# Kernel tuning notes

Measured on AMD Instinct MI355X. Metric: run time of the kernel, lower is better.

## Reference

```python
import jax, jax.numpy as jnp
import numpy as np
from itertools import combinations

DIM = 3
METRIC = np.array([1.0, 1.0, 1.0], dtype=np.float32)
KERNEL_SIZE = 7
C_IN, C_OUT = 32, 32
HIDDEN = 64
NUM_LAYERS = 4
N_GRID = KERNEL_SIZE ** DIM


def _build_cayley(dim, metric):
    blades = [()] + [c for r in range(1, dim + 1) for c in combinations(range(dim), r)]
    idx = {b: i for i, b in enumerate(blades)}
    n = len(blades)
    C = np.zeros((n, n, n), dtype=np.float32)
    for i, a in enumerate(blades):
        for j, b in enumerate(blades):
            arr = list(a) + list(b)
            sign = 1.0
            changed = True
            while changed:
                changed = False
                t = 0
                while t < len(arr) - 1:
                    if arr[t] == arr[t + 1]:
                        sign *= metric[arr[t]]
                        del arr[t:t + 2]
                        changed = True
                        break
                    if arr[t] > arr[t + 1]:
                        arr[t], arr[t + 1] = arr[t + 1], arr[t]
                        sign = -sign
                        changed = True
                    t += 1
            C[i, j, idx[tuple(arr)]] = sign
    grades = np.array([len(b) for b in blades])
    return C, grades

_C_LRO, GRADES = _build_cayley(DIM, METRIC)
CAYLEY = np.transpose(_C_LRO, (0, 2, 1))  # [left, out, right] (CEGNN convention)
N_BLADES = CAYLEY.shape[0]
N_GRADES = DIM + 1

# nonzero grade-triple paths of the Cayley tensor and blade-level path-id lookup
_gp = np.zeros((N_GRADES,) * 3, dtype=bool)
for a in range(N_GRADES):
    for b in range(N_GRADES):
        for c in range(N_GRADES):
            _gp[a, b, c] = np.any(CAYLEY[np.ix_(GRADES == a, GRADES == b, GRADES == c)] != 0)
PATHS = np.argwhere(_gp)
P = len(PATHS)
assert P == 20  # product_paths_sum for Cl(3,0)
_pid = -np.ones((N_GRADES,) * 3, dtype=np.int64)
for p, (a, b, c) in enumerate(PATHS):
    _pid[a, b, c] = p
BLADE_PID = _pid[GRADES[:, None, None], GRADES[None, :, None], GRADES[None, None, :]]
BLADE_PID = np.where(BLADE_PID < 0, P, BLADE_PID)  # P -> zero slot

# centered relative-position grid, (N, 1, dim)
_ax = np.arange(KERNEL_SIZE, dtype=np.float32) - (KERNEL_SIZE - 1) / 2.0
_grid = np.stack(np.meshgrid(*([_ax] * DIM), indexing='ij'), axis=-1).reshape(-1, DIM)
REL_POS = jnp.asarray(_grid[:, None, :])
CAYLEY_J = jnp.asarray(CAYLEY)
GRADE_ONEHOT = jnp.asarray((GRADES[:, None] == np.arange(N_GRADES)[None, :]).astype(np.float32))
FACTOR = 1.0 / np.sqrt(float(KERNEL_SIZE ** DIM))
BLADES_OF = {g: np.where(GRADES == g)[0] for g in range(N_GRADES)}


def embed_grade(x, g):
    out = jnp.zeros(x.shape[:-1] + (N_BLADES,), x.dtype)
    return out.at[..., BLADES_OF[g]].set(x)


def expand_paths(w):
    # (..., P) grade-path weights -> (..., B, B, B) blade-level weights
    wz = jnp.concatenate([w, jnp.zeros(w.shape[:-1] + (1,), w.dtype)], axis=-1)
    return wz[..., BLADE_PID]


def mv_linear(x, W, b):
    # grade-wise equivariant channel mixing; x: (N,Ci,B), W: (G,Co,Ci), bias on scalar blade
    y = jnp.einsum('boi,nib->nob', W[GRADES], x)
    return y.at[:, :, 0].add(b)


def mv_silu(x, a, b):
    # gate each grade by sigmoid of its (learned-scaled) squared norm
    qg = jnp.einsum('ncb,bg->ncg', x * x, GRADE_ONEHOT)
    gate = jax.nn.sigmoid(a * qg + b)
    return x * gate[:, :, GRADES]


def gp_layer(x, w):
    # fully-connected steerable geometric product; x: (N,C,B), w: (Co,C,P)
    wc = expand_paths(w) * CAYLEY_J  # (Co, C, B, B, B)
    y = jnp.einsum('nik,oikjm,nim->noj', x, wc, x)
    return y / np.sqrt(float(x.shape[1]))


def setup_inputs() -> dict:
    key = jax.random.key(0)
    ks = jax.random.split(key, 8)
    G, B, H, Pn = N_GRADES, N_BLADES, HIDDEN, P
    rn = lambda k, s, sc: jax.random.normal(k, s, dtype=jnp.float32) * sc
    ci1 = C_IN + 1
    return {
        'condition': rn(ks[0], (C_IN, B), 1.0),
        'rel_pos_sigma': jnp.ones((1, 1, 1), jnp.float32),
        'cayley_w': rn(ks[1], (C_OUT, C_IN, Pn), 1.0 / np.sqrt(C_IN)),
        'lin0_W': rn(ks[2], (G, H, ci1), 1.0 / np.sqrt(ci1)),
        'lin0_b': jnp.zeros((H,), jnp.float32),
        'act0_a': rn(ks[3], (H, G), 0.2),
        'act0_b': jnp.zeros((H, G), jnp.float32),
        'gps_w': rn(ks[4], (NUM_LAYERS, H, H, Pn), 0.5 / np.sqrt(H)),
        'lins_W': rn(ks[5], (NUM_LAYERS - 1, G, H, H), 1.0 / np.sqrt(H)),
        'lins_b': jnp.zeros((NUM_LAYERS - 1, H), jnp.float32),
        'acts_a': rn(ks[6], (NUM_LAYERS - 1, H, G), 0.2),
        'acts_b': jnp.zeros((NUM_LAYERS - 1, H, G), jnp.float32),
        'out_W': rn(ks[7], (G, C_OUT * C_IN, H), 1.0 / np.sqrt(H)),
        'out_b': jnp.zeros((C_OUT * C_IN,), jnp.float32),
        'shell_sigma': jnp.ones((1, C_OUT, C_IN, B), jnp.float32),
    }


def reference(condition, rel_pos_sigma, cayley_w, lin0_W, lin0_b, act0_a, act0_b,
              gps_w, lins_W, lins_b, acts_a, acts_b, out_W, out_b, shell_sigma):
    metric = jnp.asarray(METRIC)
    q = jnp.sum(metric * REL_POS * REL_POS, axis=-1, keepdims=True)  # (N,1,1)
    scalar = jnp.exp(-q / (2.0 * rel_pos_sigma ** 2))
    x = embed_grade(scalar, 0) + embed_grade(REL_POS, 1)  # (N,1,B)
    cond = jnp.broadcast_to(condition[None], (N_GRID,) + condition.shape)
    x = jnp.concatenate([x, cond], axis=1)  # (N, c_in+1, B)
    # kernel network: CEGNN blocks [MVLinear -> MVSiLU -> steerable geometric product]
    h = gp_layer(mv_silu(mv_linear(x, lin0_W, lin0_b), act0_a, act0_b), gps_w[0])
    for l in range(NUM_LAYERS - 1):
        h = gp_layer(mv_silu(mv_linear(h, lins_W[l], lins_b[l]), acts_a[l], acts_b[l]), gps_w[l + 1])
    k = mv_linear(h, out_W, out_b).reshape(N_GRID, C_OUT, C_IN, N_BLADES)
    # per-(c_out,c_in,blade) scalar radial shell
    shell = jnp.exp(-q.reshape(N_GRID, 1, 1, 1) / (shell_sigma ** 2))
    k = k * shell * FACTOR
    # kernel head: sparse weighted-Cayley contraction
    wc = expand_paths(cayley_w) * CAYLEY_J  # (c_out, c_in, B, B, B)
    K = jnp.einsum('noik,oiklm->olimn', k, wc)
    return K.reshape(C_OUT * N_BLADES, C_IN * N_BLADES, KERNEL_SIZE, KERNEL_SIZE, KERNEL_SIZE)
```

## Files before the change

kernel.cpp:

```cpp
#include <hip/hip_runtime.h>
#include <math.h>

#define NB 8
#define NGRID 343
#define HID 64
#define NPATH 20

struct Tab {
  int prod_idx[8][8];
  int prod_sgn[8][8];
  int pid[4][4][4];
  int grade[8];
  int kk_idx[8][8];
  int kk_sgn[8][8];
};

constexpr Tab make_tab() {
  Tab t{};
  int mask[8]  = {0,1,2,4,3,5,6,7};
  int idxof[8] = {0,1,2,4,3,5,6,7};
  for (int k = 0; k < 8; ++k) {
    int g = 0;
    for (int b = 0; b < 3; ++b) g += (mask[k] >> b) & 1;
    t.grade[k] = g;
  }
  for (int k = 0; k < 8; ++k)
    for (int m = 0; m < 8; ++m) {
      int A = mask[k], B = mask[m];
      t.prod_idx[k][m] = idxof[A ^ B];
      int c = 0;
      for (int i = 0; i < 3; ++i)
        if ((B >> i) & 1)
          for (int j = i + 1; j < 3; ++j)
            if ((A >> j) & 1) c++;
      t.prod_sgn[k][m] = (c & 1) ? -1 : 1;
    }
  int pc = 0;
  for (int a = 0; a < 4; ++a)
    for (int b = 0; b < 4; ++b)
      for (int c = 0; c < 4; ++c) {
        bool ok = false;
        for (int k = 0; k < 8; ++k)
          for (int m = 0; m < 8; ++m)
            if (t.grade[k] == a && t.grade[m] == c &&
                t.grade[t.prod_idx[k][m]] == b)
              ok = true;
        t.pid[a][b][c] = ok ? pc++ : NPATH;
      }
  for (int l = 0; l < 8; ++l)
    for (int m = 0; m < 8; ++m)
      for (int k = 0; k < 8; ++k)
        if (t.prod_idx[k][m] == l) {
          t.kk_idx[l][m] = k;
          t.kk_sgn[l][m] = t.prod_sgn[k][m];
        }
  return t;
}
constexpr Tab TB = make_tab();

#define OFF_LIN0T 0
#define OFF_LINST 8448
#define OFF_GPST  57600
#define OFF_OUTWT 385280
#define OFF_KWS   647424

__global__ void ccs_prep_kernel(const float* __restrict__ lin0_W,
                                const float* __restrict__ lins_W,
                                const float* __restrict__ gps_w,
                                const float* __restrict__ out_W,
                                float* __restrict__ ws) {
  const int TOT = 8448 + 49152 + 327680 + 262144;
  for (int d = blockIdx.x * blockDim.x + threadIdx.x; d < TOT;
       d += gridDim.x * blockDim.x) {
    float v;
    if (d < 8448) {
      int idx = d;
      int hh = idx & 63, ch = (idx >> 6) % 33, g = (idx >> 6) / 33;
      v = lin0_W[(g * 64 + hh) * 33 + ch];
    } else if (d < 8448 + 49152) {
      int idx = d - OFF_LINST;
      int hh = idx & 63, i = (idx >> 6) & 63, g = (idx >> 12) & 3, l = idx >> 14;
      v = lins_W[((l * 4 + g) * 64 + hh) * 64 + i];
    } else if (d < 8448 + 49152 + 327680) {
      int idx = d - OFF_GPST;
      int o = idx & 63, p = (idx >> 6) % 20, i = ((idx >> 6) / 20) & 63,
          l = idx / 81920;
      v = gps_w[((l * 64 + o) * 64 + i) * 20 + p];
    } else {
      int idx = d - OFF_OUTWT;
      int oc = idx & 1023, i = (idx >> 10) & 63, g = idx >> 16;
      v = out_W[(g * 1024 + oc) * 64 + i];
    }
    ws[d] = v;
  }
}

__launch_bounds__(256)
__global__ void ccs_net_kernel(const float* __restrict__ condition,
                               const float* __restrict__ rel_pos_sigma,
                               const float* __restrict__ lin0_b,
                               const float* __restrict__ act0_a,
                               const float* __restrict__ act0_b,
                               const float* __restrict__ lins_b,
                               const float* __restrict__ acts_a,
                               const float* __restrict__ acts_b,
                               const float* __restrict__ out_b,
                               const float* __restrict__ shell_sigma,
                               const float* __restrict__ ws,
                               float* __restrict__ kws) {
  const float* lin0t = ws + OFF_LIN0T;
  const float* linst = ws + OFF_LINST;
  const float* gpst  = ws + OFF_GPST;
  const float* outwt = ws + OFF_OUTWT;

  __shared__ float xb[33 * 8];
  __shared__ float F0[64 * 8];
  __shared__ float F1[64 * 8];
  __shared__ float part[4 * 64 * 8];

  const int n = blockIdx.x;
  const int tid = threadIdx.x;
  const int iz = n % 7, iy = (n / 7) % 7, ix = n / 49;
  const float px = (float)ix - 3.f, py = (float)iy - 3.f, pz = (float)iz - 3.f;
  const float q = px * px + py * py + pz * pz;
  const float sig = rel_pos_sigma[0];
  const float scal = expf(-q / (2.f * sig * sig));

  for (int t = tid; t < 264; t += 256) {
    int ch = t >> 3, b = t & 7;
    float v;
    if (ch == 0)
      v = (b == 0) ? scal : (b == 1) ? px : (b == 2) ? py : (b == 3) ? pz : 0.f;
    else
      v = condition[(ch - 1) * 8 + b];
    xb[t] = v;
  }
  __syncthreads();

  const int hh = tid & 63;
  const int brow = tid >> 6;

  #pragma unroll
  for (int rep = 0; rep < 2; ++rep) {
    int b = brow + 4 * rep;
    int g = TB.grade[b];
    float acc = (b == 0) ? lin0_b[hh] : 0.f;
    const float* wrow = lin0t + g * 33 * 64 + hh;
    #pragma unroll
    for (int ch = 0; ch < 33; ++ch)
      acc = fmaf(wrow[ch * 64], xb[ch * 8 + b], acc);
    F0[hh * 8 + b] = acc;
  }
  __syncthreads();

  auto silu = [&](const float* src, float* dst, const float* aa,
                  const float* bb) {
    #pragma unroll
    for (int rep = 0; rep < 2; ++rep) {
      int b = brow + 4 * rep;
      int g = TB.grade[b];
      int s0 = (g == 0) ? 0 : (g == 1) ? 1 : (g == 2) ? 4 : 7;
      int cnt = (g == 0 || g == 3) ? 1 : 3;
      float qg = 0.f;
      for (int u = 0; u < cnt; ++u) {
        float v = src[hh * 8 + s0 + u];
        qg = fmaf(v, v, qg);
      }
      float z = fmaf(aa[hh * 4 + g], qg, bb[hh * 4 + g]);
      float gate = 1.f / (1.f + expf(-z));
      dst[hh * 8 + b] = src[hh * 8 + b] * gate;
    }
  };

  auto lin = [&](const float* src, float* dst, const float* wt,
                 const float* bias) {
    #pragma unroll
    for (int rep = 0; rep < 2; ++rep) {
      int b = brow + 4 * rep;
      int g = TB.grade[b];
      float acc = (b == 0) ? bias[hh] : 0.f;
      const float* wrow = wt + g * 64 * 64 + hh;
      #pragma unroll
      for (int i = 0; i < 64; ++i)
        acc = fmaf(wrow[i * 64], src[i * 8 + b], acc);
      dst[hh * 8 + b] = acc;
    }
  };

  auto gp = [&](const float* src, float* dst, const float* wl) {
    const int o = tid & 63;
    const int isub = tid >> 6;
    float facc[8];
    #pragma unroll
    for (int j = 0; j < 8; ++j) facc[j] = 0.f;
    for (int it = 0; it < 16; ++it) {
      int i = isub * 16 + it;
      float x8[8];
      #pragma unroll
      for (int b = 0; b < 8; ++b) x8[b] = src[i * 8 + b];
      const float* wb = wl + i * 20 * 64 + o;
      float wp[20];
      #pragma unroll
      for (int p = 0; p < 20; ++p) wp[p] = wb[p * 64];
      #pragma unroll
      for (int k = 0; k < 8; ++k) {
        #pragma unroll
        for (int m = 0; m < 8; ++m) {
          const int j = TB.prod_idx[k][m];
          const int p = TB.pid[TB.grade[k]][TB.grade[j]][TB.grade[m]];
          float tp = x8[k] * x8[m];
          if (TB.prod_sgn[k][m] > 0)
            facc[j] = fmaf(tp, wp[p], facc[j]);
          else
            facc[j] = fmaf(-tp, wp[p], facc[j]);
        }
      }
    }
    #pragma unroll
    for (int j = 0; j < 8; ++j) part[(isub * 64 + o) * 8 + j] = facc[j];
    __syncthreads();
    #pragma unroll
    for (int rep = 0; rep < 2; ++rep) {
      int idx = tid + rep * 256;
      float s = part[idx] + part[idx + 512] + part[idx + 1024] +
                part[idx + 1536];
      dst[idx] = s * 0.125f;
    }
    __syncthreads();
  };

  silu(F0, F1, act0_a, act0_b);
  __syncthreads();
  gp(F1, F0, gpst + 0);

  float* f = F0;
  float* g_ = F1;
  for (int l = 0; l < 3; ++l) {
    lin(f, g_, linst + l * 16384, lins_b + l * 64);
    __syncthreads();
    silu(g_, f, acts_a + l * 256, acts_b + l * 256);
    __syncthreads();
    gp(f, g_, gpst + (l + 1) * 81920);
    float* t = f; f = g_; g_ = t;
  }

  const float FACTOR = 1.0f / sqrtf(343.0f);
  #pragma unroll
  for (int r = 0; r < 4; ++r) {
    int oc = tid + r * 256;
    float acc[8];
    #pragma unroll
    for (int b = 0; b < 8; ++b) acc[b] = 0.f;
    acc[0] = out_b[oc];
    #pragma unroll 8
    for (int i = 0; i < 64; ++i) {
      float w0 = outwt[(0 * 64 + i) * 1024 + oc];
      float w1 = outwt[(1 * 64 + i) * 1024 + oc];
      float w2 = outwt[(2 * 64 + i) * 1024 + oc];
      float w3 = outwt[(3 * 64 + i) * 1024 + oc];
      const float* h = f + i * 8;
      acc[0] = fmaf(w0, h[0], acc[0]);
      acc[1] = fmaf(w1, h[1], acc[1]);
      acc[2] = fmaf(w1, h[2], acc[2]);
      acc[3] = fmaf(w1, h[3], acc[3]);
      acc[4] = fmaf(w2, h[4], acc[4]);
      acc[5] = fmaf(w2, h[5], acc[5]);
      acc[6] = fmaf(w2, h[6], acc[6]);
      acc[7] = fmaf(w3, h[7], acc[7]);
    }
    float out8[8];
    #pragma unroll
    for (int b = 0; b < 8; ++b) {
      float ss = shell_sigma[oc * 8 + b];
      out8[b] = acc[b] * expf(-q / (ss * ss)) * FACTOR;
    }
    float4* dst = (float4*)(kws + ((size_t)oc * 343 + n) * 8);
    dst[0] = make_float4(out8[0], out8[1], out8[2], out8[3]);
    dst[1] = make_float4(out8[4], out8[5], out8[6], out8[7]);
  }
}

__launch_bounds__(64)
__global__ void ccs_expand_kernel(const float* __restrict__ cayley_w,
                                  const float* __restrict__ kws,
                                  float* __restrict__ out) {
  const int oi = blockIdx.x;
  const int o = oi >> 5, i = oi & 31;
  const int n = blockIdx.y * 64 + threadIdx.x;
  if (n >= NGRID) return;
  float cw[20];
  #pragma unroll
  for (int p = 0; p < 20; ++p) cw[p] = cayley_w[oi * 20 + p];
  const float* kp = kws + ((size_t)oi * 343 + n) * 8;
  float k8[8];
  #pragma unroll
  for (int b = 0; b < 8; ++b) k8[b] = kp[b];
  #pragma unroll
  for (int l = 0; l < 8; ++l) {
    #pragma unroll
    for (int m = 0; m < 8; ++m) {
      const int kk = TB.kk_idx[l][m];
      const int p = TB.pid[TB.grade[kk]][TB.grade[l]][TB.grade[m]];
      float v = k8[kk] * cw[p];
      if (TB.kk_sgn[l][m] < 0) v = -v;
      out[((size_t)((o * 8 + l) * 256 + i * 8 + m)) * 343 + n] = v;
    }
  }
}

extern "C" void kernel_launch(void* const* d_in, const int* in_sizes, int n_in,
                              void* d_out, int out_size, void* d_ws,
                              size_t ws_size, hipStream_t stream) {
  const float* condition     = (const float*)d_in[0];
  const float* rel_pos_sigma = (const float*)d_in[1];
  const float* cayley_w      = (const float*)d_in[2];
  const float* lin0_W        = (const float*)d_in[3];
  const float* lin0_b        = (const float*)d_in[4];
  const float* act0_a        = (const float*)d_in[5];
  const float* act0_b        = (const float*)d_in[6];
  const float* gps_w         = (const float*)d_in[7];
  const float* lins_W        = (const float*)d_in[8];
  const float* lins_b        = (const float*)d_in[9];
  const float* acts_a        = (const float*)d_in[10];
  const float* acts_b        = (const float*)d_in[11];
  const float* out_W         = (const float*)d_in[12];
  const float* out_b         = (const float*)d_in[13];
  const float* shell_sigma   = (const float*)d_in[14];

  float* ws = (float*)d_ws;
  float* kws = ws + OFF_KWS;
  float* out = (float*)d_out;

  ccs_prep_kernel<<<dim3(640), dim3(256), 0, stream>>>(lin0_W, lins_W, gps_w,
                                                       out_W, ws);
  ccs_net_kernel<<<dim3(343), dim3(256), 0, stream>>>(
      condition, rel_pos_sigma, lin0_b, act0_a, act0_b, lins_b, acts_a, acts_b,
      out_b, shell_sigma, ws, kws);
  ccs_expand_kernel<<<dim3(1024, 6), dim3(64), 0, stream>>>(cayley_w, kws, out);
}
```

Before: 220.9 us.

## Widen net blocks to 1024 threads, exploit product symmetry, restage expand through LDS

The network kernel now runs 1024 threads per grid point. It splits the geometric-product reduction 16 ways and pairs symmetric (k,m)/(m,k) terms to roughly halve the FMAs. Weights are read as float4 through new blade-major shared layouts, and the linear weights are read directly in their original layout. The kws intermediate is made n-major, and the expand kernel stages one (o,i) slice in padded shared memory so each block writes whole 343-element output rows. The larger blocks add sync cost and idle half of the threads in the 512-wide phases.

```diff
diff --git a/kernel.cpp b/kernel.cpp
--- a/kernel.cpp
+++ b/kernel.cpp
@@ -1,9 +1,7 @@
 #include <hip/hip_runtime.h>
 #include <math.h>
 
-#define NB 8
 #define NGRID 343
-#define HID 64
 #define NPATH 20
 
 struct Tab {
@@ -58,65 +56,62 @@
 }
 constexpr Tab TB = make_tab();
 
+__device__ __forceinline__ int gradeOf(int b) {
+  return (b == 0) ? 0 : (b < 4) ? 1 : (b < 7) ? 2 : 3;
+}
+
 #define OFF_LIN0T 0
-#define OFF_LINST 8448
-#define OFF_GPST  57600
-#define OFF_OUTWT 385280
-#define OFF_KWS   647424
+#define OFF_GPST  8448
+#define OFF_OUTWT 336128
+#define OFF_KWS   598272
 
 __global__ void ccs_prep_kernel(const float* __restrict__ lin0_W,
-                                const float* __restrict__ lins_W,
                                 const float* __restrict__ gps_w,
                                 const float* __restrict__ out_W,
                                 float* __restrict__ ws) {
-  const int TOT = 8448 + 49152 + 327680 + 262144;
+  const int TOT = 8448 + 327680 + 262144;
   for (int d = blockIdx.x * blockDim.x + threadIdx.x; d < TOT;
        d += gridDim.x * blockDim.x) {
     float v;
     if (d < 8448) {
-      int idx = d;
-      int hh = idx & 63, ch = (idx >> 6) % 33, g = (idx >> 6) / 33;
+      int hh = d & 63, ch = (d >> 6) % 33, g = (d >> 6) / 33;
       v = lin0_W[(g * 64 + hh) * 33 + ch];
-    } else if (d < 8448 + 49152) {
-      int idx = d - OFF_LINST;
-      int hh = idx & 63, i = (idx >> 6) & 63, g = (idx >> 12) & 3, l = idx >> 14;
-      v = lins_W[((l * 4 + g) * 64 + hh) * 64 + i];
-    } else if (d < 8448 + 49152 + 327680) {
+    } else if (d < OFF_OUTWT) {
       int idx = d - OFF_GPST;
-      int o = idx & 63, p = (idx >> 6) % 20, i = ((idx >> 6) / 20) & 63,
-          l = idx / 81920;
-      v = gps_w[((l * 64 + o) * 64 + i) * 20 + p];
+      int p = idx % 20, r = idx / 20;
+      int o = r & 63, i = (r >> 6) & 63, l = r >> 12;
+      v = gps_w[(((size_t)l * 64 + o) * 64 + i) * 20 + p];
     } else {
       int idx = d - OFF_OUTWT;
-      int oc = idx & 1023, i = (idx >> 10) & 63, g = idx >> 16;
+      int g = idx & 3, i = (idx >> 2) & 63, oc = idx >> 8;
       v = out_W[(g * 1024 + oc) * 64 + i];
     }
     ws[d] = v;
   }
 }
 
-__launch_bounds__(256)
-__global__ void ccs_net_kernel(const float* __restrict__ condition,
-                               const float* __restrict__ rel_pos_sigma,
-                               const float* __restrict__ lin0_b,
-                               const float* __restrict__ act0_a,
-                               const float* __restrict__ act0_b,
-                               const float* __restrict__ lins_b,
-                               const float* __restrict__ acts_a,
-                               const float* __restrict__ acts_b,
-                               const float* __restrict__ out_b,
-                               const float* __restrict__ shell_sigma,
-                               const float* __restrict__ ws,
-                               float* __restrict__ kws) {
+__global__ __launch_bounds__(1024, 4)
+void ccs_net_kernel(const float* __restrict__ condition,
+                    const float* __restrict__ rel_pos_sigma,
+                    const float* __restrict__ lin0_b,
+                    const float* __restrict__ act0_a,
+                    const float* __restrict__ act0_b,
+                    const float* __restrict__ lins_W,
+                    const float* __restrict__ lins_b,
+                    const float* __restrict__ acts_a,
+                    const float* __restrict__ acts_b,
+                    const float* __restrict__ out_b,
+                    const float* __restrict__ shell_sigma,
+                    const float* __restrict__ ws,
+                    float* __restrict__ kws) {
   const float* lin0t = ws + OFF_LIN0T;
-  const float* linst = ws + OFF_LINST;
   const float* gpst  = ws + OFF_GPST;
   const float* outwt = ws + OFF_OUTWT;
 
-  __shared__ float xb[33 * 8];
-  __shared__ float F0[64 * 8];
-  __shared__ float F1[64 * 8];
-  __shared__ float part[4 * 64 * 8];
+  __shared__ __align__(16) float xb[264];
+  __shared__ __align__(16) float F0[512];
+  __shared__ __align__(16) float F1[512];
+  __shared__ __align__(16) float part[8192];
 
   const int n = blockIdx.x;
   const int tid = threadIdx.x;
@@ -126,184 +121,203 @@
   const float sig = rel_pos_sigma[0];
   const float scal = expf(-q / (2.f * sig * sig));
 
-  for (int t = tid; t < 264; t += 256) {
-    int ch = t >> 3, b = t & 7;
+  if (tid < 264) {
+    int ch = tid >> 3, b = tid & 7;
     float v;
     if (ch == 0)
       v = (b == 0) ? scal : (b == 1) ? px : (b == 2) ? py : (b == 3) ? pz : 0.f;
     else
       v = condition[(ch - 1) * 8 + b];
-    xb[t] = v;
+    xb[tid] = v;
   }
   __syncthreads();
 
   const int hh = tid & 63;
-  const int brow = tid >> 6;
-
-  #pragma unroll
-  for (int rep = 0; rep < 2; ++rep) {
-    int b = brow + 4 * rep;
-    int g = TB.grade[b];
-    float acc = (b == 0) ? lin0_b[hh] : 0.f;
-    const float* wrow = lin0t + g * 33 * 64 + hh;
+  const int bb = (tid >> 6) & 7;
+  const bool act512 = tid < 512;
+
+  if (act512) {
+    int g = gradeOf(bb);
+    float acc = (bb == 0) ? lin0_b[hh] : 0.f;
+    const float* wrow = lin0t + g * (33 * 64) + hh;
     #pragma unroll
     for (int ch = 0; ch < 33; ++ch)
-      acc = fmaf(wrow[ch * 64], xb[ch * 8 + b], acc);
-    F0[hh * 8 + b] = acc;
+      acc = fmaf(wrow[ch * 64], xb[ch * 8 + bb], acc);
+    F0[bb * 64 + hh] = acc;
   }
   __syncthreads();
 
   auto silu = [&](const float* src, float* dst, const float* aa,
-                  const float* bb) {
-    #pragma unroll
-    for (int rep = 0; rep < 2; ++rep) {
-      int b = brow + 4 * rep;
-      int g = TB.grade[b];
+                  const float* ab) {
+    if (act512) {
+      int g = gradeOf(bb);
       int s0 = (g == 0) ? 0 : (g == 1) ? 1 : (g == 2) ? 4 : 7;
       int cnt = (g == 0 || g == 3) ? 1 : 3;
       float qg = 0.f;
       for (int u = 0; u < cnt; ++u) {
-        float v = src[hh * 8 + s0 + u];
+        float v = src[(s0 + u) * 64 + hh];
         qg = fmaf(v, v, qg);
       }
-      float z = fmaf(aa[hh * 4 + g], qg, bb[hh * 4 + g]);
+      float z = fmaf(aa[hh * 4 + g], qg, ab[hh * 4 + g]);
       float gate = 1.f / (1.f + expf(-z));
-      dst[hh * 8 + b] = src[hh * 8 + b] * gate;
+      dst[bb * 64 + hh] = src[bb * 64 + hh] * gate;
     }
   };
 
-  auto lin = [&](const float* src, float* dst, const float* wt,
+  auto lin = [&](const float* src, float* dst, const float* wl,
                  const float* bias) {
-    #pragma unroll
-    for (int rep = 0; rep < 2; ++rep) {
-      int b = brow + 4 * rep;
-      int g = TB.grade[b];
-      float acc = (b == 0) ? bias[hh] : 0.f;
-      const float* wrow = wt + g * 64 * 64 + hh;
-      #pragma unroll
-      for (int i = 0; i < 64; ++i)
-        acc = fmaf(wrow[i * 64], src[i * 8 + b], acc);
-      dst[hh * 8 + b] = acc;
+    if (act512) {
+      int g = gradeOf(bb);
+      float acc = (bb == 0) ? bias[hh] : 0.f;
+      const float4* wr = (const float4*)(wl + ((size_t)g * 64 + hh) * 64);
+      #pragma unroll
+      for (int u = 0; u < 16; ++u) {
+        float4 w = wr[u];
+        const float* s = src + bb * 64 + u * 4;
+        acc = fmaf(w.x, s[0], acc);
+        acc = fmaf(w.y, s[1], acc);
+        acc = fmaf(w.z, s[2], acc);
+        acc = fmaf(w.w, s[3], acc);
+      }
+      dst[bb * 64 + hh] = acc;
     }
   };
 
-  auto gp = [&](const float* src, float* dst, const float* wl) {
+  auto gp = [&](const float* src, float* dst, const float* wl, bool imaj) {
     const int o = tid & 63;
     const int isub = tid >> 6;
     float facc[8];
     #pragma unroll
     for (int j = 0; j < 8; ++j) facc[j] = 0.f;
-    for (int it = 0; it < 16; ++it) {
-      int i = isub * 16 + it;
+    #pragma unroll
+    for (int it = 0; it < 4; ++it) {
+      const int i = isub * 4 + it;
       float x8[8];
       #pragma unroll
-      for (int b = 0; b < 8; ++b) x8[b] = src[i * 8 + b];
-      const float* wb = wl + i * 20 * 64 + o;
-      float wp[20];
-      #pragma unroll
-      for (int p = 0; p < 20; ++p) wp[p] = wb[p * 64];
+      for (int b = 0; b < 8; ++b) x8[b] = src[b * 64 + i];
+      float4 w4[5];
+      const float4* wb = (const float4*)(wl + ((size_t)i * 64 + o) * 20);
+      #pragma unroll
+      for (int u = 0; u < 5; ++u) w4[u] = wb[u];
+      const float* wp = (const float*)w4;
+      #pragma unroll
+      for (int k = 0; k < 8; ++k) {
+        const int p = TB.pid[TB.grade[k]][0][TB.grade[k]];
+        float tp = x8[k] * x8[k];
+        facc[0] = fmaf(TB.prod_sgn[k][k] > 0 ? tp : -tp, wp[p], facc[0]);
+      }
       #pragma unroll
       for (int k = 0; k < 8; ++k) {
         #pragma unroll
-        for (int m = 0; m < 8; ++m) {
-          const int j = TB.prod_idx[k][m];
-          const int p = TB.pid[TB.grade[k]][TB.grade[j]][TB.grade[m]];
-          float tp = x8[k] * x8[m];
-          if (TB.prod_sgn[k][m] > 0)
-            facc[j] = fmaf(tp, wp[p], facc[j]);
-          else
-            facc[j] = fmaf(-tp, wp[p], facc[j]);
+        for (int m = k + 1; m < 8; ++m) {
+          const int j  = TB.prod_idx[k][m];
+          const int p1 = TB.pid[TB.grade[k]][TB.grade[j]][TB.grade[m]];
+          const int p2 = TB.pid[TB.grade[m]][TB.grade[j]][TB.grade[k]];
+          const float w1 = (TB.prod_sgn[k][m] > 0) ? wp[p1] : -wp[p1];
+          const float w2 = (TB.prod_sgn[m][k] > 0) ? wp[p2] : -wp[p2];
+          facc[j] = fmaf(x8[k] * x8[m], w1 + w2, facc[j]);
         }
       }
     }
     #pragma unroll
-    for (int j = 0; j < 8; ++j) part[(isub * 64 + o) * 8 + j] = facc[j];
+    for (int j = 0; j < 8; ++j) part[(j * 16 + isub) * 64 + o] = facc[j];
     __syncthreads();
-    #pragma unroll
-    for (int rep = 0; rep < 2; ++rep) {
-      int idx = tid + rep * 256;
-      float s = part[idx] + part[idx + 512] + part[idx + 1024] +
-                part[idx + 1536];
-      dst[idx] = s * 0.125f;
+    if (act512) {
+      const int o2 = tid & 63, j2 = tid >> 6;
+      float s = 0.f;
+      #pragma unroll
+      for (int u = 0; u < 16; ++u) s += part[(j2 * 16 + u) * 64 + o2];
+      s *= 0.125f;
+      if (imaj)
+        dst[o2 * 8 + j2] = s;
+      else
+        dst[j2 * 64 + o2] = s;
     }
     __syncthreads();
   };
 
   silu(F0, F1, act0_a, act0_b);
   __syncthreads();
-  gp(F1, F0, gpst + 0);
+  gp(F1, F0, gpst + 0, false);
 
   float* f = F0;
   float* g_ = F1;
+  #pragma unroll 1
   for (int l = 0; l < 3; ++l) {
-    lin(f, g_, linst + l * 16384, lins_b + l * 64);
+    lin(f, g_, lins_W + (size_t)l * 16384, lins_b + l * 64);
     __syncthreads();
     silu(g_, f, acts_a + l * 256, acts_b + l * 256);
     __syncthreads();
-    gp(f, g_, gpst + (l + 1) * 81920);
+    gp(f, g_, gpst + (size_t)(l + 1) * 81920, l == 2);
     float* t = f; f = g_; g_ = t;
   }
 
   const float FACTOR = 1.0f / sqrtf(343.0f);
+  const int oc = tid;
+  float acc[8];
   #pragma unroll
-  for (int r = 0; r < 4; ++r) {
-    int oc = tid + r * 256;
-    float acc[8];
-    #pragma unroll
-    for (int b = 0; b < 8; ++b) acc[b] = 0.f;
-    acc[0] = out_b[oc];
-    #pragma unroll 8
-    for (int i = 0; i < 64; ++i) {
-      float w0 = outwt[(0 * 64 + i) * 1024 + oc];
-      float w1 = outwt[(1 * 64 + i) * 1024 + oc];
-      float w2 = outwt[(2 * 64 + i) * 1024 + oc];
-      float w3 = outwt[(3 * 64 + i) * 1024 + oc];
-      const float* h = f + i * 8;
-      acc[0] = fmaf(w0, h[0], acc[0]);
-      acc[1] = fmaf(w1, h[1], acc[1]);
-      acc[2] = fmaf(w1, h[2], acc[2]);
-      acc[3] = fmaf(w1, h[3], acc[3]);
-      acc[4] = fmaf(w2, h[4], acc[4]);
-      acc[5] = fmaf(w2, h[5], acc[5]);
-      acc[6] = fmaf(w2, h[6], acc[6]);
-      acc[7] = fmaf(w3, h[7], acc[7]);
-    }
-    float out8[8];
-    #pragma unroll
-    for (int b = 0; b < 8; ++b) {
-      float ss = shell_sigma[oc * 8 + b];
-      out8[b] = acc[b] * expf(-q / (ss * ss)) * FACTOR;
-    }
-    float4* dst = (float4*)(kws + ((size_t)oc * 343 + n) * 8);
-    dst[0] = make_float4(out8[0], out8[1], out8[2], out8[3]);
-    dst[1] = make_float4(out8[4], out8[5], out8[6], out8[7]);
-  }
-}
-
-__launch_bounds__(64)
-__global__ void ccs_expand_kernel(const float* __restrict__ cayley_w,
-                                  const float* __restrict__ kws,
-                                  float* __restrict__ out) {
+  for (int b = 0; b < 8; ++b) acc[b] = 0.f;
+  acc[0] = out_b[oc];
+  const float4* wv = (const float4*)(outwt + (size_t)oc * 256);
+  #pragma unroll 8
+  for (int i = 0; i < 64; ++i) {
+    float4 w = wv[i];
+    const float4* hp = (const float4*)(f + i * 8);
+    float4 h0 = hp[0], h1 = hp[1];
+    acc[0] = fmaf(w.x, h0.x, acc[0]);
+    acc[1] = fmaf(w.y, h0.y, acc[1]);
+    acc[2] = fmaf(w.y, h0.z, acc[2]);
+    acc[3] = fmaf(w.y, h0.w, acc[3]);
+    acc[4] = fmaf(w.z, h1.x, acc[4]);
+    acc[5] = fmaf(w.z, h1.y, acc[5]);
+    acc[6] = fmaf(w.z, h1.z, acc[6]);
+    acc[7] = fmaf(w.w, h1.w, acc[7]);
+  }
+  float4 s0 = ((const float4*)(shell_sigma + oc * 8))[0];
+  float4 s1 = ((const float4*)(shell_sigma + oc * 8))[1];
+  float o8[8];
+  o8[0] = acc[0] * expf(-q / (s0.x * s0.x)) * FACTOR;
+  o8[1] = acc[1] * expf(-q / (s0.y * s0.y)) * FACTOR;
+  o8[2] = acc[2] * expf(-q / (s0.z * s0.z)) * FACTOR;
+  o8[3] = acc[3] * expf(-q / (s0.w * s0.w)) * FACTOR;
+  o8[4] = acc[4] * expf(-q / (s1.x * s1.x)) * FACTOR;
+  o8[5] = acc[5] * expf(-q / (s1.y * s1.y)) * FACTOR;
+  o8[6] = acc[6] * expf(-q / (s1.z * s1.z)) * FACTOR;
+  o8[7] = acc[7] * expf(-q / (s1.w * s1.w)) * FACTOR;
+  float4* dst = (float4*)(kws + ((size_t)n * 1024 + oc) * 8);
+  dst[0] = make_float4(o8[0], o8[1], o8[2], o8[3]);
+  dst[1] = make_float4(o8[4], o8[5], o8[6], o8[7]);
+}
+
+__global__ __launch_bounds__(256)
+void ccs_expand_kernel(const float* __restrict__ cayley_w,
+                       const float* __restrict__ kws,
+                       float* __restrict__ out) {
   const int oi = blockIdx.x;
   const int o = oi >> 5, i = oi & 31;
-  const int n = blockIdx.y * 64 + threadIdx.x;
-  if (n >= NGRID) return;
+  const int tid = threadIdx.x;
+  __shared__ float sk[343 * 9];
+
+  for (int idx = tid; idx < 686; idx += 256) {
+    int nn = idx >> 1, h = (idx & 1) * 4;
+    float4 v = *(const float4*)(kws + ((size_t)nn * 1024 + oi) * 8 + h);
+    float* s = sk + nn * 9 + h;
+    s[0] = v.x; s[1] = v.y; s[2] = v.z; s[3] = v.w;
+  }
   float cw[20];
   #pragma unroll
   for (int p = 0; p < 20; ++p) cw[p] = cayley_w[oi * 20 + p];
-  const float* kp = kws + ((size_t)oi * 343 + n) * 8;
-  float k8[8];
-  #pragma unroll
-  for (int b = 0; b < 8; ++b) k8[b] = kp[b];
+  __syncthreads();
+
   #pragma unroll
   for (int l = 0; l < 8; ++l) {
     #pragma unroll
     for (int m = 0; m < 8; ++m) {
       const int kk = TB.kk_idx[l][m];
       const int p = TB.pid[TB.grade[kk]][TB.grade[l]][TB.grade[m]];
-      float v = k8[kk] * cw[p];
-      if (TB.kk_sgn[l][m] < 0) v = -v;
-      out[((size_t)((o * 8 + l) * 256 + i * 8 + m)) * 343 + n] = v;
+      const float wv = (TB.kk_sgn[l][m] > 0) ? cw[p] : -cw[p];
+      float* orow = out + ((size_t)((o * 8 + l) * 256 + i * 8 + m)) * 343;
+      for (int c = tid; c < 343; c += 256) orow[c] = sk[c * 9 + kk] * wv;
     }
   }
 }
@@ -331,10 +345,10 @@
   float* kws = ws + OFF_KWS;
   float* out = (float*)d_out;
 
-  ccs_prep_kernel<<<dim3(640), dim3(256), 0, stream>>>(lin0_W, lins_W, gps_w,
-                                                       out_W, ws);
-  ccs_net_kernel<<<dim3(343), dim3(256), 0, stream>>>(
-      condition, rel_pos_sigma, lin0_b, act0_a, act0_b, lins_b, acts_a, acts_b,
-      out_b, shell_sigma, ws, kws);
-  ccs_expand_kernel<<<dim3(1024, 6), dim3(64), 0, stream>>>(cayley_w, kws, out);
-}
+  ccs_prep_kernel<<<dim3(640), dim3(256), 0, stream>>>(lin0_W, gps_w, out_W,
+                                                       ws);
+  ccs_net_kernel<<<dim3(343), dim3(1024), 0, stream>>>(
+      condition, rel_pos_sigma, lin0_b, act0_a, act0_b, lins_W, lins_b, acts_a,
+      acts_b, out_b, shell_sigma, ws, kws);
+  ccs_expand_kernel<<<dim3(1024), dim3(256), 0, stream>>>(cayley_w, kws, out);
+}
```

New measurement: 262.7 us. 18.9% more time.
